# Optimization experiments

Measured on AMD Instinct MI355X. Metric: run time of the kernel, lower is better.

## Reference

```python
import jax, jax.numpy as jnp
import numpy as np


def setup_inputs() -> dict:
    key = jax.random.key(0)
    k1, k2, k3 = jax.random.split(key, 3)
    T, B, C, H, W = 64, 2, 32, 32, 32
    x_seq = jax.random.normal(k1, (T, B, C, H, W), dtype=jnp.float32)
    A_kernel = jax.random.normal(k2, (C, 3, 3), dtype=jnp.float32) * 0.1
    B_kernel = jax.random.normal(k3, (C, 3, 3), dtype=jnp.float32) * 0.1
    return {"x_seq": x_seq, "A_kernel": A_kernel, "B_kernel": B_kernel}


def reference(x_seq, A_kernel, B_kernel):
    # ConvSSM recurrence h_t = A * h_{t-1} + B * x_t (circular conv via zero-padded FFT)
    # computed with an associative parallel scan in the frequency domain.
    H, W = x_seq.shape[-2], x_seq.shape[-1]
    fft_size = (2 * H, 2 * W)
    axes = (-2, -1)

    x_f = jnp.fft.rfftn(x_seq.astype(jnp.float32), s=fft_size, axes=axes)  # (T,B,C,2H,W+1) complex
    A_f = jnp.fft.rfftn(A_kernel.astype(jnp.float32), s=fft_size, axes=axes)  # (C,2H,W+1)
    B_f = jnpp_rfft = jnp.fft.rfftn(B_kernel.astype(jnp.float32), s=fft_size, axes=axes)

    # scan elements: (a_t, s_t) with a_t = A_f, s_t = B_f * X_t
    a = jnp.broadcast_to(A_f[None, None], x_f.shape)
    s = x_f * B_f[None, None]

    def combine(left, right):
        # (a1,s1) (+) (a2,s2) = (a1*a2, s1*a2 + s2); left is earlier in time
        a1, s1 = left
        a2, s2 = right
        return (a1 * a2, s1 * a2 + s2)

    _, h_f = jax.lax.associative_scan(combine, (a, s), axis=0)

    h = jnp.fft.irfftn(h_f, s=fft_size, axes=axes)  # (T,B,C,2H,2W) real
    return h[..., :H, :W].astype(x_seq.dtype)
```

## Files before the change

kernel.cpp:

```cpp
#include <hip/hip_runtime.h>


constexpr int T_STEPS = 64;
constexpr int B_DIM   = 2;
constexpr int C_DIM   = 32;
constexpr int HW      = 32;
constexpr int N       = 64;
constexpr int NIMG    = B_DIM * C_DIM;
constexpr int MH      = T_STEPS / 2;
constexpr int HSTR    = 68;
constexpr int GSZ     = 36 * 36;
constexpr int USZ     = HW * HW;

__global__ __launch_bounds__(256)
void convssm_pass1c(const float* __restrict__ x_seq,
                    const float* __restrict__ A_k,
                    const float* __restrict__ B_k,
                    float* __restrict__ U,
                    float* __restrict__ G)
{
    __shared__ float xe[32][33];
    __shared__ float xo[32][33];
    __shared__ float ue[34][35];

    const int blk = blockIdx.x;
    const int m   = blk >> 6;
    const int bc  = blk & 63;
    const int c   = bc & 31;
    const int tid = threadIdx.x;

    float a[9], bw[9];
#pragma unroll
    for (int i = 0; i < 9; ++i) { a[i] = A_k[c * 9 + i]; bw[i] = B_k[c * 9 + i]; }

    const float* xE = x_seq + ((size_t)(2 * m)     * NIMG + bc) * (HW * HW);
    const float* xO = x_seq + ((size_t)(2 * m + 1) * NIMG + bc) * (HW * HW);
#pragma unroll
    for (int k = 0; k < 4; ++k) {
        int i = tid + k * 256;
        int y = i >> 5, xx = i & 31;
        xe[y][xx] = xE[i];
        xo[y][xx] = xO[i];
    }
    __syncthreads();

    float* Ug = U + (size_t)(bc * MH + m) * USZ;
    for (int i = tid; i < 34 * 34; i += 256) {
        int y = i / 34, xx = i - y * 34;
        float v = 0.0f;
#pragma unroll
        for (int ky = 0; ky < 3; ++ky) {
            int yy = y - ky;
            if (yy < 0 || yy >= 32) continue;
#pragma unroll
            for (int kx = 0; kx < 3; ++kx) {
                int xs = xx - kx;
                if (xs < 0 || xs >= 32) continue;
                v += bw[ky * 3 + kx] * xe[yy][xs];
            }
        }
        ue[y][xx] = v;
        if (y < 32 && xx < 32) Ug[y * 32 + xx] = v;
    }
    __syncthreads();

    float* Gg = G + (size_t)(bc * MH + m) * GSZ;
    for (int i = tid; i < GSZ; i += 256) {
        int y = i / 36, xx = i - y * 36;
        float v = 0.0f;
#pragma unroll
        for (int ky = 0; ky < 3; ++ky) {
#pragma unroll
            for (int kx = 0; kx < 3; ++kx) {
                int yy = y - ky, xs = xx - kx;
                if (yy >= 0 && yy < 32 && xs >= 0 && xs < 32)
                    v += bw[ky * 3 + kx] * xo[yy][xs];
                if (yy >= 0 && yy < 34 && xs >= 0 && xs < 34)
                    v += a[ky * 3 + kx] * ue[yy][xs];
            }
        }
        Gg[i] = v;
    }
}

__global__ __launch_bounds__(512, 2)
void convssm_scan4(const float* __restrict__ U,
                   const float* __restrict__ G,
                   const float* __restrict__ A_k,
                   float* __restrict__ out)
{
    __shared__ __align__(16) float hbuf[2][N * HSTR];

    const int bc  = blockIdx.x;
    const int c   = bc & 31;
    const int tid = threadIdx.x;
    const int g   = tid & 15;
    const int s   = tid >> 4;
    const int y0  = s * 2;
    const int xc  = g * 4;
    const int xlo = (xc + 60) & 63;

    float a[9];
#pragma unroll
    for (int i = 0; i < 9; ++i) a[i] = A_k[c * 9 + i];

    float a2[5][5];
#pragma unroll
    for (int p = 0; p < 5; ++p) {
#pragma unroll
        for (int q = 0; q < 5; ++q) {
            float v = 0.0f;
#pragma unroll
            for (int ky = 0; ky < 3; ++ky) {
                int py = p - ky;
                if (py < 0 || py > 2) continue;
#pragma unroll
                for (int kx = 0; kx < 3; ++kx) {
                    int qx = q - kx;
                    if (qx < 0 || qx > 2) continue;
                    v += a[ky * 3 + kx] * a[py * 3 + qx];
                }
            }
            a2[p][q] = v;
        }
    }

    for (int i = tid; i < N * HSTR; i += 512) hbuf[0][i] = 0.0f;

    const bool gok   = (y0 <= 34) && (xc <= 32);
    const bool cropw = (y0 < HW);
    const bool crop  = cropw && (xc < HW);

    const float* Ub = U + (size_t)bc * MH * USZ + y0 * HW + xc;
    const float* Gb = G + (size_t)bc * MH * GSZ + y0 * 36 + xc;

    const float4 z4 = make_float4(0.f, 0.f, 0.f, 0.f);
    float4 gc0 = z4, gc1 = z4, uc0 = z4, uc1 = z4;
    if (gok) {
        gc0 = *(const float4*)(Gb);
        gc1 = *(const float4*)(Gb + 36);
    }
    if (crop) {
        uc0 = *(const float4*)(Ub);
        uc1 = *(const float4*)(Ub + HW);
    }

    float* hold = &hbuf[0][0];
    float* hnew = &hbuf[1][0];
    float* ob   = out + (size_t)bc * (HW * HW);
    const size_t tstr = (size_t)NIMG * (HW * HW);

    __syncthreads();

    for (int m = 0; m < MH; ++m) {
        float4 gn0 = z4, gn1 = z4, un0 = z4, un1 = z4;
        if (m + 1 < MH) {
            if (gok) {
                const float* p = Gb + (size_t)(m + 1) * GSZ;
                gn0 = *(const float4*)(p);
                gn1 = *(const float4*)(p + 36);
            }
            if (crop) {
                const float* p = Ub + (size_t)(m + 1) * USZ;
                un0 = *(const float4*)(p);
                un1 = *(const float4*)(p + HW);
            }
        }

        float w[6][8];
#pragma unroll
        for (int i = 0; i < 6; ++i) {
            const int R = (y0 - 4 + i) & 63;
            const float4 lo = *(const float4*)(hold + R * HSTR + xlo);
            const float4 hi = *(const float4*)(hold + R * HSTR + xc);
            w[i][0] = lo.x; w[i][1] = lo.y; w[i][2] = lo.z; w[i][3] = lo.w;
            w[i][4] = hi.x; w[i][5] = hi.y; w[i][6] = hi.z; w[i][7] = hi.w;
        }

        float acc[2][4];
        acc[0][0] = gc0.x; acc[0][1] = gc0.y; acc[0][2] = gc0.z; acc[0][3] = gc0.w;
        acc[1][0] = gc1.x; acc[1][1] = gc1.y; acc[1][2] = gc1.z; acc[1][3] = gc1.w;
#pragma unroll
        for (int r = 0; r < 2; ++r) {
#pragma unroll
            for (int p = 0; p < 5; ++p) {
                const int i = r + 4 - p;
#pragma unroll
                for (int q = 0; q < 5; ++q) {
                    const float cf = a2[p][q];
#pragma unroll
                    for (int j = 0; j < 4; ++j)
                        acc[r][j] += cf * w[i][4 + j - q];
                }
            }
        }

        *(float4*)(hnew + y0 * HSTR + xc) =
            make_float4(acc[0][0], acc[0][1], acc[0][2], acc[0][3]);
        *(float4*)(hnew + (y0 + 1) * HSTR + xc) =
            make_float4(acc[1][0], acc[1][1], acc[1][2], acc[1][3]);

        if (cropw) {
            float E[2][4];
            E[0][0] = uc0.x; E[0][1] = uc0.y; E[0][2] = uc0.z; E[0][3] = uc0.w;
            E[1][0] = uc1.x; E[1][1] = uc1.y; E[1][2] = uc1.z; E[1][3] = uc1.w;
#pragma unroll
            for (int r = 0; r < 2; ++r) {
#pragma unroll
                for (int ky = 0; ky < 3; ++ky) {
                    const int i = r + 4 - ky;
#pragma unroll
                    for (int kx = 0; kx < 3; ++kx) {
                        const float cf = a[ky * 3 + kx];
#pragma unroll
                        for (int j = 0; j < 4; ++j)
                            E[r][j] += cf * w[i][4 + j - kx];
                    }
                }
            }
            if (crop) {
                float* oe = ob + (size_t)(2 * m) * tstr;
                float* oo = oe + tstr;
#pragma unroll
                for (int r = 0; r < 2; ++r) {
                    *(float4*)(oe + (y0 + r) * HW + xc) =
                        make_float4(E[r][0], E[r][1], E[r][2], E[r][3]);
                    *(float4*)(oo + (y0 + r) * HW + xc) =
                        make_float4(acc[r][0], acc[r][1], acc[r][2], acc[r][3]);
                }
            }
        }

        __syncthreads();

        float* tmp = hold; hold = hnew; hnew = tmp;
        gc0 = gn0; gc1 = gn1;
        uc0 = un0; uc1 = un1;
    }
}

__global__ __launch_bounds__(256)
void convssm_scan_fused(const float* __restrict__ x_seq,
                        const float* __restrict__ A_k,
                        const float* __restrict__ B_k,
                        float* __restrict__ out)
{
    __shared__ float h0[N][N];
    __shared__ float h1[N][N];
    __shared__ float xs[N][N];

    const int bc = blockIdx.x;
    const int b  = bc >> 5;
    const int c  = bc & 31;
    const int tid = threadIdx.x;
    const int x   = tid & 63;
    const int y0  = (tid >> 6) << 4;

    float a[9], bw[9];
#pragma unroll
    for (int i = 0; i < 9; ++i) { a[i] = A_k[c*9+i]; bw[i] = B_k[c*9+i]; }
#pragma unroll
    for (int r = 0; r < 16; ++r) { h0[y0+r][x] = 0.f; xs[y0+r][x] = 0.f; }

    float (*hold)[N] = h0;
    float (*hnew)[N] = h1;
    const int xm1 = (x + 63) & 63, xm2 = (x + 62) & 63;
    const size_t img = (size_t)HW*HW, tstr = (size_t)NIMG*img;
    const float* xbase = x_seq + ((size_t)b*C_DIM + c)*img;
    float* obase = out + ((size_t)b*C_DIM + c)*img;
    const bool loader = (x < HW);

    for (int t = 0; t < T_STEPS; ++t) {
        if (loader) {
#pragma unroll
            for (int r = 0; r < 16; ++r) {
                int yy = y0 + r;
                if (yy < HW) xs[yy][x] = xbase[(size_t)t*tstr + yy*HW + x];
            }
        }
        __syncthreads();
        const int ym1 = (y0 + N - 1) & 63, ym2 = (y0 + N - 2) & 63;
        float hr1c0 = hold[ym1][x], hr1c1 = hold[ym1][xm1], hr1c2 = hold[ym1][xm2];
        float hr2c0 = hold[ym2][x], hr2c1 = hold[ym2][xm1], hr2c2 = hold[ym2][xm2];
        float sr1c0 = xs[ym1][x], sr1c1 = xs[ym1][xm1], sr1c2 = xs[ym1][xm2];
        float sr2c0 = xs[ym2][x], sr2c1 = xs[ym2][xm1], sr2c2 = xs[ym2][xm2];
#pragma unroll
        for (int r = 0; r < 16; ++r) {
            const int yy = y0 + r;
            float hr0c0 = hold[yy][x], hr0c1 = hold[yy][xm1], hr0c2 = hold[yy][xm2];
            float sr0c0 = xs[yy][x], sr0c1 = xs[yy][xm1], sr0c2 = xs[yy][xm2];
            float v = a[0]*hr0c0 + a[1]*hr0c1 + a[2]*hr0c2
                    + a[3]*hr1c0 + a[4]*hr1c1 + a[5]*hr1c2
                    + a[6]*hr2c0 + a[7]*hr2c1 + a[8]*hr2c2
                    + bw[0]*sr0c0 + bw[1]*sr0c1 + bw[2]*sr0c2
                    + bw[3]*sr1c0 + bw[4]*sr1c1 + bw[5]*sr1c2
                    + bw[6]*sr2c0 + bw[7]*sr2c1 + bw[8]*sr2c2;
            hnew[yy][x] = v;
            if (yy < HW && x < HW) obase[(size_t)t*tstr + yy*HW + x] = v;
            hr2c0=hr1c0; hr2c1=hr1c1; hr2c2=hr1c2;
            hr1c0=hr0c0; hr1c1=hr0c1; hr1c2=hr0c2;
            sr2c0=sr1c0; sr2c1=sr1c1; sr2c2=sr1c2;
            sr1c0=sr0c0; sr1c1=sr0c1; sr1c2=sr0c2;
        }
        __syncthreads();
        float (*tmp)[N] = hold; hold = hnew; hnew = tmp;
    }
}

extern "C" void kernel_launch(void* const* d_in, const int* in_sizes, int n_in,
                              void* d_out, int out_size, void* d_ws, size_t ws_size,
                              hipStream_t stream)
{
    const float* x_seq = (const float*)d_in[0];
    const float* A_k   = (const float*)d_in[1];
    const float* B_k   = (const float*)d_in[2];
    float* out = (float*)d_out;

    const size_t needU = (size_t)NIMG * MH * USZ;
    const size_t needG = (size_t)NIMG * MH * GSZ;
    const size_t need  = (needU + needG) * sizeof(float);

    if (ws_size >= need) {
        float* U = (float*)d_ws;
        float* G = U + needU;
        convssm_pass1c<<<dim3(MH * NIMG), dim3(256), 0, stream>>>(
            x_seq, A_k, B_k, U, G);
        convssm_scan4<<<dim3(NIMG), dim3(512), 0, stream>>>(
            U, G, A_k, out);
    } else {
        convssm_scan_fused<<<dim3(NIMG), dim3(256), 0, stream>>>(
            x_seq, A_k, B_k, out);
    }
}
```

Before: 60.71 us.

## Widen scan to one row per thread and vectorize pass-1 loads and stores

```diff
diff --git a/kernel.cpp b/kernel.cpp
--- a/kernel.cpp
+++ b/kernel.cpp
@@ -12,16 +12,20 @@
 constexpr int GSZ     = 36 * 36;
 constexpr int USZ     = HW * HW;
 
+__device__ __forceinline__ float rfl(float v) {
+    return __int_as_float(__builtin_amdgcn_readfirstlane(__float_as_int(v)));
+}
+
 __global__ __launch_bounds__(256)
-void convssm_pass1c(const float* __restrict__ x_seq,
+void convssm_pass1d(const float* __restrict__ x_seq,
                     const float* __restrict__ A_k,
                     const float* __restrict__ B_k,
                     float* __restrict__ U,
                     float* __restrict__ G)
 {
-    __shared__ float xe[32][33];
-    __shared__ float xo[32][33];
-    __shared__ float ue[34][35];
+    __shared__ __align__(16) float xe[32][36];
+    __shared__ __align__(16) float xo[32][36];
+    __shared__ __align__(16) float ue[34][36];
 
     const int blk = blockIdx.x;
     const int m   = blk >> 6;
@@ -33,18 +37,16 @@
 #pragma unroll
     for (int i = 0; i < 9; ++i) { a[i] = A_k[c * 9 + i]; bw[i] = B_k[c * 9 + i]; }
 
-    const float* xE = x_seq + ((size_t)(2 * m)     * NIMG + bc) * (HW * HW);
-    const float* xO = x_seq + ((size_t)(2 * m + 1) * NIMG + bc) * (HW * HW);
-#pragma unroll
-    for (int k = 0; k < 4; ++k) {
-        int i = tid + k * 256;
-        int y = i >> 5, xx = i & 31;
-        xe[y][xx] = xE[i];
-        xo[y][xx] = xO[i];
+    const float4* xE = (const float4*)(x_seq + ((size_t)(2 * m)     * NIMG + bc) * (HW * HW));
+    const float4* xO = (const float4*)(x_seq + ((size_t)(2 * m + 1) * NIMG + bc) * (HW * HW));
+    {
+        const int y  = tid >> 3;
+        const int x4 = (tid & 7) * 4;
+        *(float4*)&xe[y][x4] = xE[tid];
+        *(float4*)&xo[y][x4] = xO[tid];
     }
     __syncthreads();
 
-    float* Ug = U + (size_t)(bc * MH + m) * USZ;
     for (int i = tid; i < 34 * 34; i += 256) {
         int y = i / 34, xx = i - y * 34;
         float v = 0.0f;
@@ -60,31 +62,44 @@
             }
         }
         ue[y][xx] = v;
-        if (y < 32 && xx < 32) Ug[y * 32 + xx] = v;
     }
     __syncthreads();
 
+    float* Ug = U + (size_t)(bc * MH + m) * USZ;
+    {
+        const int y  = tid >> 3;
+        const int x4 = (tid & 7) * 4;
+        *(float4*)(Ug + y * HW + x4) = *(const float4*)&ue[y][x4];
+    }
+
     float* Gg = G + (size_t)(bc * MH + m) * GSZ;
-    for (int i = tid; i < GSZ; i += 256) {
-        int y = i / 36, xx = i - y * 36;
-        float v = 0.0f;
-#pragma unroll
-        for (int ky = 0; ky < 3; ++ky) {
-#pragma unroll
-            for (int kx = 0; kx < 3; ++kx) {
-                int yy = y - ky, xs = xx - kx;
-                if (yy >= 0 && yy < 32 && xs >= 0 && xs < 32)
-                    v += bw[ky * 3 + kx] * xo[yy][xs];
-                if (yy >= 0 && yy < 34 && xs >= 0 && xs < 34)
-                    v += a[ky * 3 + kx] * ue[yy][xs];
-            }
-        }
-        Gg[i] = v;
-    }
-}
-
-__global__ __launch_bounds__(512, 2)
-void convssm_scan4(const float* __restrict__ U,
+    for (int i4 = tid; i4 < 324; i4 += 256) {
+        const int y  = i4 / 9;
+        const int x0 = (i4 - y * 9) * 4;
+        float r[4];
+#pragma unroll
+        for (int j = 0; j < 4; ++j) {
+            const int xx = x0 + j;
+            float v = 0.0f;
+#pragma unroll
+            for (int ky = 0; ky < 3; ++ky) {
+#pragma unroll
+                for (int kx = 0; kx < 3; ++kx) {
+                    int yy = y - ky, xs = xx - kx;
+                    if (yy >= 0 && yy < 32 && xs >= 0 && xs < 32)
+                        v += bw[ky * 3 + kx] * xo[yy][xs];
+                    if (yy >= 0 && yy < 34 && xs >= 0 && xs < 34)
+                        v += a[ky * 3 + kx] * ue[yy][xs];
+                }
+            }
+            r[j] = v;
+        }
+        *(float4*)(Gg + y * 36 + x0) = make_float4(r[0], r[1], r[2], r[3]);
+    }
+}
+
+__global__ __launch_bounds__(1024)
+void convssm_scan5(const float* __restrict__ U,
                    const float* __restrict__ G,
                    const float* __restrict__ A_k,
                    float* __restrict__ out)
@@ -95,16 +110,15 @@
     const int c   = bc & 31;
     const int tid = threadIdx.x;
     const int g   = tid & 15;
-    const int s   = tid >> 4;
-    const int y0  = s * 2;
+    const int y   = tid >> 4;
     const int xc  = g * 4;
     const int xlo = (xc + 60) & 63;
 
-    float a[9];
-#pragma unroll
-    for (int i = 0; i < 9; ++i) a[i] = A_k[c * 9 + i];
-
-    float a2[5][5];
+    float af[9];
+#pragma unroll
+    for (int i = 0; i < 9; ++i) af[i] = A_k[c * 9 + i];
+
+    float a2f[25];
 #pragma unroll
     for (int p = 0; p < 5; ++p) {
 #pragma unroll
@@ -118,124 +132,101 @@
                 for (int kx = 0; kx < 3; ++kx) {
                     int qx = q - kx;
                     if (qx < 0 || qx > 2) continue;
-                    v += a[ky * 3 + kx] * a[py * 3 + qx];
+                    v += af[ky * 3 + kx] * af[py * 3 + qx];
                 }
             }
-            a2[p][q] = v;
-        }
-    }
-
-    for (int i = tid; i < N * HSTR; i += 512) hbuf[0][i] = 0.0f;
-
-    const bool gok   = (y0 <= 34) && (xc <= 32);
-    const bool cropw = (y0 < HW);
+            a2f[p * 5 + q] = v;
+        }
+    }
+#pragma unroll
+    for (int i = 0; i < 25; ++i) a2f[i] = rfl(a2f[i]);
+#pragma unroll
+    for (int i = 0; i < 9; ++i)  af[i]  = rfl(af[i]);
+
+    for (int i = tid; i < N * HSTR; i += 1024) hbuf[0][i] = 0.0f;
+
+    const bool cropw = (y < HW);
     const bool crop  = cropw && (xc < HW);
-
-    const float* Ub = U + (size_t)bc * MH * USZ + y0 * HW + xc;
-    const float* Gb = G + (size_t)bc * MH * GSZ + y0 * 36 + xc;
+    const bool gok   = (y < 36) && (xc <= 32);
+
+    const float* Ub = U + (size_t)bc * MH * USZ + y * HW + xc;
+    const float* Gb = G + (size_t)bc * MH * GSZ + y * 36 + xc;
 
     const float4 z4 = make_float4(0.f, 0.f, 0.f, 0.f);
-    float4 gc0 = z4, gc1 = z4, uc0 = z4, uc1 = z4;
-    if (gok) {
-        gc0 = *(const float4*)(Gb);
-        gc1 = *(const float4*)(Gb + 36);
-    }
-    if (crop) {
-        uc0 = *(const float4*)(Ub);
-        uc1 = *(const float4*)(Ub + HW);
-    }
+    float4 gc = z4, uc = z4;
+    if (gok)  gc = *(const float4*)(Gb);
+    if (crop) uc = *(const float4*)(Ub);
 
     float* hold = &hbuf[0][0];
     float* hnew = &hbuf[1][0];
     float* ob   = out + (size_t)bc * (HW * HW);
     const size_t tstr = (size_t)NIMG * (HW * HW);
 
+    float4 acc = z4;
+
     __syncthreads();
 
     for (int m = 0; m < MH; ++m) {
-        float4 gn0 = z4, gn1 = z4, un0 = z4, un1 = z4;
+        float4 gn = z4, un = z4;
         if (m + 1 < MH) {
-            if (gok) {
-                const float* p = Gb + (size_t)(m + 1) * GSZ;
-                gn0 = *(const float4*)(p);
-                gn1 = *(const float4*)(p + 36);
-            }
-            if (crop) {
-                const float* p = Ub + (size_t)(m + 1) * USZ;
-                un0 = *(const float4*)(p);
-                un1 = *(const float4*)(p + HW);
-            }
-        }
-
-        float w[6][8];
-#pragma unroll
-        for (int i = 0; i < 6; ++i) {
-            const int R = (y0 - 4 + i) & 63;
-            const float4 lo = *(const float4*)(hold + R * HSTR + xlo);
-            const float4 hi = *(const float4*)(hold + R * HSTR + xc);
+            if (gok)  gn = *(const float4*)(Gb + (size_t)(m + 1) * GSZ);
+            if (crop) un = *(const float4*)(Ub + (size_t)(m + 1) * USZ);
+        }
+
+        float w[5][8];
+#pragma unroll
+        for (int i = 0; i < 5; ++i) {
+            const int rr = (y + 60 + i) & 63;
+            const float4 lo = *(const float4*)(hold + rr * HSTR + xlo);
             w[i][0] = lo.x; w[i][1] = lo.y; w[i][2] = lo.z; w[i][3] = lo.w;
-            w[i][4] = hi.x; w[i][5] = hi.y; w[i][6] = hi.z; w[i][7] = hi.w;
-        }
-
-        float acc[2][4];
-        acc[0][0] = gc0.x; acc[0][1] = gc0.y; acc[0][2] = gc0.z; acc[0][3] = gc0.w;
-        acc[1][0] = gc1.x; acc[1][1] = gc1.y; acc[1][2] = gc1.z; acc[1][3] = gc1.w;
-#pragma unroll
-        for (int r = 0; r < 2; ++r) {
-#pragma unroll
-            for (int p = 0; p < 5; ++p) {
-                const int i = r + 4 - p;
-#pragma unroll
-                for (int q = 0; q < 5; ++q) {
-                    const float cf = a2[p][q];
+            if (i < 4) {
+                const float4 hi = *(const float4*)(hold + rr * HSTR + xc);
+                w[i][4] = hi.x; w[i][5] = hi.y; w[i][6] = hi.z; w[i][7] = hi.w;
+            }
+        }
+        w[4][4] = acc.x; w[4][5] = acc.y; w[4][6] = acc.z; w[4][7] = acc.w;
+
+        float o[4] = { gc.x, gc.y, gc.z, gc.w };
+#pragma unroll
+        for (int p = 0; p < 5; ++p) {
+            const int i = 4 - p;
+#pragma unroll
+            for (int q = 0; q < 5; ++q) {
+                const float cf = a2f[p * 5 + q];
+#pragma unroll
+                for (int j = 0; j < 4; ++j)
+                    o[j] += cf * w[i][4 + j - q];
+            }
+        }
+        const float4 accn = make_float4(o[0], o[1], o[2], o[3]);
+
+        if (cropw) {
+            float e[4] = { uc.x, uc.y, uc.z, uc.w };
+#pragma unroll
+            for (int ky = 0; ky < 3; ++ky) {
+                const int i = 4 - ky;
+#pragma unroll
+                for (int kx = 0; kx < 3; ++kx) {
+                    const float cf = af[ky * 3 + kx];
 #pragma unroll
                     for (int j = 0; j < 4; ++j)
-                        acc[r][j] += cf * w[i][4 + j - q];
-                }
-            }
-        }
-
-        *(float4*)(hnew + y0 * HSTR + xc) =
-            make_float4(acc[0][0], acc[0][1], acc[0][2], acc[0][3]);
-        *(float4*)(hnew + (y0 + 1) * HSTR + xc) =
-            make_float4(acc[1][0], acc[1][1], acc[1][2], acc[1][3]);
-
-        if (cropw) {
-            float E[2][4];
-            E[0][0] = uc0.x; E[0][1] = uc0.y; E[0][2] = uc0.z; E[0][3] = uc0.w;
-            E[1][0] = uc1.x; E[1][1] = uc1.y; E[1][2] = uc1.z; E[1][3] = uc1.w;
-#pragma unroll
-            for (int r = 0; r < 2; ++r) {
-#pragma unroll
-                for (int ky = 0; ky < 3; ++ky) {
-                    const int i = r + 4 - ky;
-#pragma unroll
-                    for (int kx = 0; kx < 3; ++kx) {
-                        const float cf = a[ky * 3 + kx];
-#pragma unroll
-                        for (int j = 0; j < 4; ++j)
-                            E[r][j] += cf * w[i][4 + j - kx];
-                    }
+                        e[j] += cf * w[i][4 + j - kx];
                 }
             }
             if (crop) {
                 float* oe = ob + (size_t)(2 * m) * tstr;
-                float* oo = oe + tstr;
-#pragma unroll
-                for (int r = 0; r < 2; ++r) {
-                    *(float4*)(oe + (y0 + r) * HW + xc) =
-                        make_float4(E[r][0], E[r][1], E[r][2], E[r][3]);
-                    *(float4*)(oo + (y0 + r) * HW + xc) =
-                        make_float4(acc[r][0], acc[r][1], acc[r][2], acc[r][3]);
-                }
-            }
-        }
+                *(float4*)(oe + y * HW + xc) = make_float4(e[0], e[1], e[2], e[3]);
+                *(float4*)(oe + tstr + y * HW + xc) = accn;
+            }
+        }
+
+        *(float4*)(hnew + y * HSTR + xc) = accn;
 
         __syncthreads();
 
         float* tmp = hold; hold = hnew; hnew = tmp;
-        gc0 = gn0; gc1 = gn1;
-        uc0 = un0; uc1 = un1;
+        acc = accn;
+        gc = gn; uc = un;
     }
 }
 
@@ -323,9 +314,9 @@
     if (ws_size >= need) {
         float* U = (float*)d_ws;
         float* G = U + needU;
-        convssm_pass1c<<<dim3(MH * NIMG), dim3(256), 0, stream>>>(
+        convssm_pass1d<<<dim3(MH * NIMG), dim3(256), 0, stream>>>(
             x_seq, A_k, B_k, U, G);
-        convssm_scan4<<<dim3(NIMG), dim3(512), 0, stream>>>(
+        convssm_scan5<<<dim3(NIMG), dim3(1024), 0, stream>>>(
             U, G, A_k, out);
     } else {
         convssm_scan_fused<<<dim3(NIMG), dim3(256), 0, stream>>>(
```

Result: slower. 65.78 us (median of 4 runs) (+8.4%).

## Use packed FMA, DPP lane shifts and register-resident rows in the scan kernel

Applied to the files above, without the earlier changes.

```diff
diff --git a/kernel.cpp b/kernel.cpp
--- a/kernel.cpp
+++ b/kernel.cpp
@@ -8,20 +8,36 @@
 constexpr int N       = 64;
 constexpr int NIMG    = B_DIM * C_DIM;
 constexpr int MH      = T_STEPS / 2;
+constexpr int MT      = MH + 1;
 constexpr int HSTR    = 68;
 constexpr int GSZ     = 36 * 36;
 constexpr int USZ     = HW * HW;
 
+typedef float f2 __attribute__((ext_vector_type(2)));
+
+__device__ __forceinline__ f2 fma2(f2 a, f2 b, f2 c) {
+    return __builtin_elementwise_fma(a, b, c);
+}
+
+__device__ __forceinline__ float rfl(float v) {
+    return __int_as_float(__builtin_amdgcn_readfirstlane(__float_as_int(v)));
+}
+
+__device__ __forceinline__ float ror1(float x) {
+    return __int_as_float(__builtin_amdgcn_update_dpp(
+        0, __float_as_int(x), 0x121, 0xF, 0xF, false));
+}
+
 __global__ __launch_bounds__(256)
-void convssm_pass1c(const float* __restrict__ x_seq,
+void convssm_pass1e(const float* __restrict__ x_seq,
                     const float* __restrict__ A_k,
                     const float* __restrict__ B_k,
                     float* __restrict__ U,
                     float* __restrict__ G)
 {
-    __shared__ float xe[32][33];
-    __shared__ float xo[32][33];
-    __shared__ float ue[34][35];
+    __shared__ __align__(16) float xe[32][36];
+    __shared__ __align__(16) float xo[32][36];
+    __shared__ __align__(16) float ue[34][36];
 
     const int blk = blockIdx.x;
     const int m   = blk >> 6;
@@ -29,62 +45,85 @@
     const int c   = bc & 31;
     const int tid = threadIdx.x;
 
+    float* Ug = U + (size_t)(bc * MT + m) * USZ;
+    float* Gg = G + (size_t)(bc * MT + m) * GSZ;
+
+    if (m == MH) {
+        const float4 z4 = make_float4(0.f, 0.f, 0.f, 0.f);
+        *(float4*)(Ug + tid * 4) = z4;
+        for (int i4 = tid; i4 < 324; i4 += 256)
+            *(float4*)(Gg + i4 * 4) = z4;
+        return;
+    }
+
     float a[9], bw[9];
 #pragma unroll
     for (int i = 0; i < 9; ++i) { a[i] = A_k[c * 9 + i]; bw[i] = B_k[c * 9 + i]; }
 
-    const float* xE = x_seq + ((size_t)(2 * m)     * NIMG + bc) * (HW * HW);
-    const float* xO = x_seq + ((size_t)(2 * m + 1) * NIMG + bc) * (HW * HW);
-#pragma unroll
-    for (int k = 0; k < 4; ++k) {
-        int i = tid + k * 256;
-        int y = i >> 5, xx = i & 31;
-        xe[y][xx] = xE[i];
-        xo[y][xx] = xO[i];
+    const float4* xE = (const float4*)(x_seq + ((size_t)(2 * m)     * NIMG + bc) * (HW * HW));
+    const float4* xO = (const float4*)(x_seq + ((size_t)(2 * m + 1) * NIMG + bc) * (HW * HW));
+    {
+        const int y  = tid >> 3;
+        const int x4 = (tid & 7) * 4;
+        *(float4*)&xe[y][x4] = xE[tid];
+        *(float4*)&xo[y][x4] = xO[tid];
     }
     __syncthreads();
 
-    float* Ug = U + (size_t)(bc * MH + m) * USZ;
-    for (int i = tid; i < 34 * 34; i += 256) {
-        int y = i / 34, xx = i - y * 34;
-        float v = 0.0f;
-#pragma unroll
-        for (int ky = 0; ky < 3; ++ky) {
-            int yy = y - ky;
-            if (yy < 0 || yy >= 32) continue;
-#pragma unroll
-            for (int kx = 0; kx < 3; ++kx) {
-                int xs = xx - kx;
-                if (xs < 0 || xs >= 32) continue;
-                v += bw[ky * 3 + kx] * xe[yy][xs];
-            }
-        }
-        ue[y][xx] = v;
-        if (y < 32 && xx < 32) Ug[y * 32 + xx] = v;
+    for (int i4 = tid; i4 < 306; i4 += 256) {
+        const int y  = (i4 * 57) >> 9;
+        const int x0 = (i4 - y * 9) * 4;
+        float r[4];
+#pragma unroll
+        for (int j = 0; j < 4; ++j) {
+            const int xx = x0 + j;
+            float v = 0.0f;
+#pragma unroll
+            for (int ky = 0; ky < 3; ++ky) {
+                const int yy = y - ky;
+                if (yy < 0 || yy >= 32) continue;
+#pragma unroll
+                for (int kx = 0; kx < 3; ++kx) {
+                    const int xs = xx - kx;
+                    if (xs < 0 || xs >= 32) continue;
+                    v += bw[ky * 3 + kx] * xe[yy][xs];
+                }
+            }
+            r[j] = v;
+        }
+        *(float4*)&ue[y][x0] = make_float4(r[0], r[1], r[2], r[3]);
+        if (y < 32 && x0 < 32)
+            *(float4*)(Ug + y * HW + x0) = make_float4(r[0], r[1], r[2], r[3]);
     }
     __syncthreads();
 
-    float* Gg = G + (size_t)(bc * MH + m) * GSZ;
-    for (int i = tid; i < GSZ; i += 256) {
-        int y = i / 36, xx = i - y * 36;
-        float v = 0.0f;
-#pragma unroll
-        for (int ky = 0; ky < 3; ++ky) {
-#pragma unroll
-            for (int kx = 0; kx < 3; ++kx) {
-                int yy = y - ky, xs = xx - kx;
-                if (yy >= 0 && yy < 32 && xs >= 0 && xs < 32)
-                    v += bw[ky * 3 + kx] * xo[yy][xs];
-                if (yy >= 0 && yy < 34 && xs >= 0 && xs < 34)
-                    v += a[ky * 3 + kx] * ue[yy][xs];
-            }
-        }
-        Gg[i] = v;
+    for (int i4 = tid; i4 < 324; i4 += 256) {
+        const int y  = (i4 * 57) >> 9;
+        const int x0 = (i4 - y * 9) * 4;
+        float r[4];
+#pragma unroll
+        for (int j = 0; j < 4; ++j) {
+            const int xx = x0 + j;
+            float v = 0.0f;
+#pragma unroll
+            for (int ky = 0; ky < 3; ++ky) {
+#pragma unroll
+                for (int kx = 0; kx < 3; ++kx) {
+                    const int yy = y - ky, xs = xx - kx;
+                    if (yy >= 0 && yy < 32 && xs >= 0 && xs < 32)
+                        v += bw[ky * 3 + kx] * xo[yy][xs];
+                    if (yy >= 0 && yy < 34 && xs >= 0 && xs < 34)
+                        v += a[ky * 3 + kx] * ue[yy][xs];
+                }
+            }
+            r[j] = v;
+        }
+        *(float4*)(Gg + y * 36 + x0) = make_float4(r[0], r[1], r[2], r[3]);
     }
 }
 
 __global__ __launch_bounds__(512, 2)
-void convssm_scan4(const float* __restrict__ U,
+void convssm_scan7(const float* __restrict__ U,
                    const float* __restrict__ G,
                    const float* __restrict__ A_k,
                    float* __restrict__ out)
@@ -98,13 +137,12 @@
     const int s   = tid >> 4;
     const int y0  = s * 2;
     const int xc  = g * 4;
-    const int xlo = (xc + 60) & 63;
-
-    float a[9];
-#pragma unroll
-    for (int i = 0; i < 9; ++i) a[i] = A_k[c * 9 + i];
-
-    float a2[5][5];
+
+    float afs[9];
+#pragma unroll
+    for (int i = 0; i < 9; ++i) afs[i] = A_k[c * 9 + i];
+
+    float a2s[25];
 #pragma unroll
     for (int p = 0; p < 5; ++p) {
 #pragma unroll
@@ -112,18 +150,28 @@
             float v = 0.0f;
 #pragma unroll
             for (int ky = 0; ky < 3; ++ky) {
-                int py = p - ky;
+                const int py = p - ky;
                 if (py < 0 || py > 2) continue;
 #pragma unroll
                 for (int kx = 0; kx < 3; ++kx) {
-                    int qx = q - kx;
+                    const int qx = q - kx;
                     if (qx < 0 || qx > 2) continue;
-                    v += a[ky * 3 + kx] * a[py * 3 + qx];
+                    v += afs[ky * 3 + kx] * afs[py * 3 + qx];
                 }
             }
-            a2[p][q] = v;
-        }
-    }
+            a2s[p * 5 + q] = v;
+        }
+    }
+#pragma unroll
+    for (int i = 0; i < 25; ++i) a2s[i] = rfl(a2s[i]);
+#pragma unroll
+    for (int i = 0; i < 9; ++i)  afs[i] = rfl(afs[i]);
+
+    f2 a2d[25], afd[9];
+#pragma unroll
+    for (int i = 0; i < 25; ++i) a2d[i] = (f2){a2s[i], a2s[i]};
+#pragma unroll
+    for (int i = 0; i < 9; ++i)  afd[i] = (f2){afs[i], afs[i]};
 
     for (int i = tid; i < N * HSTR; i += 512) hbuf[0][i] = 0.0f;
 
@@ -131,8 +179,8 @@
     const bool cropw = (y0 < HW);
     const bool crop  = cropw && (xc < HW);
 
-    const float* Ub = U + (size_t)bc * MH * USZ + y0 * HW + xc;
-    const float* Gb = G + (size_t)bc * MH * GSZ + y0 * 36 + xc;
+    const float* Ub = U + (size_t)bc * MT * USZ + y0 * HW + xc;
+    const float* Gb = G + (size_t)bc * MT * GSZ + y0 * 36 + xc;
 
     const float4 z4 = make_float4(0.f, 0.f, 0.f, 0.f);
     float4 gc0 = z4, gc1 = z4, uc0 = z4, uc1 = z4;
@@ -150,90 +198,112 @@
     float* ob   = out + (size_t)bc * (HW * HW);
     const size_t tstr = (size_t)NIMG * (HW * HW);
 
+    float4 acc0 = z4, acc1 = z4;
+
     __syncthreads();
 
     for (int m = 0; m < MH; ++m) {
         float4 gn0 = z4, gn1 = z4, un0 = z4, un1 = z4;
-        if (m + 1 < MH) {
-            if (gok) {
-                const float* p = Gb + (size_t)(m + 1) * GSZ;
-                gn0 = *(const float4*)(p);
-                gn1 = *(const float4*)(p + 36);
-            }
-            if (crop) {
-                const float* p = Ub + (size_t)(m + 1) * USZ;
-                un0 = *(const float4*)(p);
-                un1 = *(const float4*)(p + HW);
-            }
-        }
-
-        float w[6][8];
+        if (gok) {
+            const float* p = Gb + (size_t)(m + 1) * GSZ;
+            gn0 = *(const float4*)(p);
+            gn1 = *(const float4*)(p + 36);
+        }
+        if (crop) {
+            const float* p = Ub + (size_t)(m + 1) * USZ;
+            un0 = *(const float4*)(p);
+            un1 = *(const float4*)(p + HW);
+        }
+
+        f2 w2[6][4], sh[6][3];
 #pragma unroll
         for (int i = 0; i < 6; ++i) {
-            const int R = (y0 - 4 + i) & 63;
-            const float4 lo = *(const float4*)(hold + R * HSTR + xlo);
-            const float4 hi = *(const float4*)(hold + R * HSTR + xc);
-            w[i][0] = lo.x; w[i][1] = lo.y; w[i][2] = lo.z; w[i][3] = lo.w;
-            w[i][4] = hi.x; w[i][5] = hi.y; w[i][6] = hi.z; w[i][7] = hi.w;
-        }
-
-        float acc[2][4];
-        acc[0][0] = gc0.x; acc[0][1] = gc0.y; acc[0][2] = gc0.z; acc[0][3] = gc0.w;
-        acc[1][0] = gc1.x; acc[1][1] = gc1.y; acc[1][2] = gc1.z; acc[1][3] = gc1.w;
-#pragma unroll
-        for (int r = 0; r < 2; ++r) {
-#pragma unroll
-            for (int p = 0; p < 5; ++p) {
-                const int i = r + 4 - p;
-#pragma unroll
-                for (int q = 0; q < 5; ++q) {
-                    const float cf = a2[p][q];
-#pragma unroll
-                    for (int j = 0; j < 4; ++j)
-                        acc[r][j] += cf * w[i][4 + j - q];
-                }
-            }
-        }
-
-        *(float4*)(hnew + y0 * HSTR + xc) =
-            make_float4(acc[0][0], acc[0][1], acc[0][2], acc[0][3]);
-        *(float4*)(hnew + (y0 + 1) * HSTR + xc) =
-            make_float4(acc[1][0], acc[1][1], acc[1][2], acc[1][3]);
+            float4 h4;
+            if (i < 4) {
+                const int rr = (y0 + 60 + i) & 63;
+                h4 = *(const float4*)(hold + rr * HSTR + xc);
+            } else {
+                h4 = (i == 4) ? acc0 : acc1;
+            }
+            w2[i][2] = (f2){h4.x, h4.y};
+            w2[i][3] = (f2){h4.z, h4.w};
+            w2[i][0] = (f2){ror1(h4.x), ror1(h4.y)};
+            w2[i][1] = (f2){ror1(h4.z), ror1(h4.w)};
+            sh[i][0] = (f2){w2[i][0].y, w2[i][1].x};
+            sh[i][1] = (f2){w2[i][1].y, w2[i][2].x};
+            sh[i][2] = (f2){w2[i][2].y, w2[i][3].x};
+        }
+
+        f2 o01 = (f2){gc0.x, gc0.y}, o23 = (f2){gc0.z, gc0.w};
+        f2 p01 = (f2){gc1.x, gc1.y}, p23 = (f2){gc1.z, gc1.w};
+#pragma unroll
+        for (int p = 0; p < 5; ++p) {
+            const int i  = 4 - p;
+            const int i2 = 5 - p;
+            const f2 c0 = a2d[p * 5 + 0], c1 = a2d[p * 5 + 1], c2 = a2d[p * 5 + 2],
+                     c3 = a2d[p * 5 + 3], c4 = a2d[p * 5 + 4];
+            o01 = fma2(c0, w2[i][2], o01);
+            o01 = fma2(c1, sh[i][1], o01);
+            o01 = fma2(c2, w2[i][1], o01);
+            o01 = fma2(c3, sh[i][0], o01);
+            o01 = fma2(c4, w2[i][0], o01);
+            o23 = fma2(c0, w2[i][3], o23);
+            o23 = fma2(c1, sh[i][2], o23);
+            o23 = fma2(c2, w2[i][2], o23);
+            o23 = fma2(c3, sh[i][1], o23);
+            o23 = fma2(c4, w2[i][1], o23);
+            p01 = fma2(c0, w2[i2][2], p01);
+            p01 = fma2(c1, sh[i2][1], p01);
+            p01 = fma2(c2, w2[i2][1], p01);
+            p01 = fma2(c3, sh[i2][0], p01);
+            p01 = fma2(c4, w2[i2][0], p01);
+            p23 = fma2(c0, w2[i2][3], p23);
+            p23 = fma2(c1, sh[i2][2], p23);
+            p23 = fma2(c2, w2[i2][2], p23);
+            p23 = fma2(c3, sh[i2][1], p23);
+            p23 = fma2(c4, w2[i2][1], p23);
+        }
+        const float4 accn0 = make_float4(o01.x, o01.y, o23.x, o23.y);
+        const float4 accn1 = make_float4(p01.x, p01.y, p23.x, p23.y);
 
         if (cropw) {
-            float E[2][4];
-            E[0][0] = uc0.x; E[0][1] = uc0.y; E[0][2] = uc0.z; E[0][3] = uc0.w;
-            E[1][0] = uc1.x; E[1][1] = uc1.y; E[1][2] = uc1.z; E[1][3] = uc1.w;
-#pragma unroll
-            for (int r = 0; r < 2; ++r) {
-#pragma unroll
-                for (int ky = 0; ky < 3; ++ky) {
-                    const int i = r + 4 - ky;
-#pragma unroll
-                    for (int kx = 0; kx < 3; ++kx) {
-                        const float cf = a[ky * 3 + kx];
-#pragma unroll
-                        for (int j = 0; j < 4; ++j)
-                            E[r][j] += cf * w[i][4 + j - kx];
-                    }
-                }
+            f2 e01 = (f2){uc0.x, uc0.y}, e23 = (f2){uc0.z, uc0.w};
+            f2 f01 = (f2){uc1.x, uc1.y}, f23 = (f2){uc1.z, uc1.w};
+#pragma unroll
+            for (int ky = 0; ky < 3; ++ky) {
+                const int i  = 4 - ky;
+                const int i2 = 5 - ky;
+                const f2 c0 = afd[ky * 3 + 0], c1 = afd[ky * 3 + 1], c2 = afd[ky * 3 + 2];
+                e01 = fma2(c0, w2[i][2], e01);
+                e01 = fma2(c1, sh[i][1], e01);
+                e01 = fma2(c2, w2[i][1], e01);
+                e23 = fma2(c0, w2[i][3], e23);
+                e23 = fma2(c1, sh[i][2], e23);
+                e23 = fma2(c2, w2[i][2], e23);
+                f01 = fma2(c0, w2[i2][2], f01);
+                f01 = fma2(c1, sh[i2][1], f01);
+                f01 = fma2(c2, w2[i2][1], f01);
+                f23 = fma2(c0, w2[i2][3], f23);
+                f23 = fma2(c1, sh[i2][2], f23);
+                f23 = fma2(c2, w2[i2][2], f23);
             }
             if (crop) {
                 float* oe = ob + (size_t)(2 * m) * tstr;
                 float* oo = oe + tstr;
-#pragma unroll
-                for (int r = 0; r < 2; ++r) {
-                    *(float4*)(oe + (y0 + r) * HW + xc) =
-                        make_float4(E[r][0], E[r][1], E[r][2], E[r][3]);
-                    *(float4*)(oo + (y0 + r) * HW + xc) =
-                        make_float4(acc[r][0], acc[r][1], acc[r][2], acc[r][3]);
-                }
-            }
-        }
+                *(float4*)(oe + y0 * HW + xc)       = make_float4(e01.x, e01.y, e23.x, e23.y);
+                *(float4*)(oe + (y0 + 1) * HW + xc) = make_float4(f01.x, f01.y, f23.x, f23.y);
+                *(float4*)(oo + y0 * HW + xc)       = accn0;
+                *(float4*)(oo + (y0 + 1) * HW + xc) = accn1;
+            }
+        }
+
+        *(float4*)(hnew + y0 * HSTR + xc)       = accn0;
+        *(float4*)(hnew + (y0 + 1) * HSTR + xc) = accn1;
 
         __syncthreads();
 
         float* tmp = hold; hold = hnew; hnew = tmp;
+        acc0 = accn0; acc1 = accn1;
         gc0 = gn0; gc1 = gn1;
         uc0 = un0; uc1 = un1;
     }
@@ -316,16 +386,16 @@
     const float* B_k   = (const float*)d_in[2];
     float* out = (float*)d_out;
 
-    const size_t needU = (size_t)NIMG * MH * USZ;
-    const size_t needG = (size_t)NIMG * MH * GSZ;
+    const size_t needU = (size_t)NIMG * MT * USZ;
+    const size_t needG = (size_t)NIMG * MT * GSZ;
     const size_t need  = (needU + needG) * sizeof(float);
 
     if (ws_size >= need) {
         float* U = (float*)d_ws;
         float* G = U + needU;
-        convssm_pass1c<<<dim3(MH * NIMG), dim3(256), 0, stream>>>(
+        convssm_pass1e<<<dim3(MT * NIMG), dim3(256), 0, stream>>>(
             x_seq, A_k, B_k, U, G);
-        convssm_scan4<<<dim3(NIMG), dim3(512), 0, stream>>>(
+        convssm_scan7<<<dim3(NIMG), dim3(512), 0, stream>>>(
             U, G, A_k, out);
     } else {
         convssm_scan_fused<<<dim3(NIMG), dim3(256), 0, stream>>>(
```

Result: slower. 66.86 us (+10.1%).
